# Kernel optimization log

Hardware: AMD Instinct MI355X
Metric: run time of the kernel (lower is better)

The kernel has to match this reference:

```python
import jax, jax.numpy as jnp
import numpy as np

N_ENT = 50000     # n_entities
C = 128           # channel
N_EDGES = 1600000 # n_edges (avg degree 32)
N_REL = 11        # n_relations; edge_type in [1, N_REL-1]
N_HOPS = 3
EPS = 1e-12       # F.normalize default eps


def setup_inputs() -> dict:
    key = jax.random.key(0)
    k1, k2, k3, k4 = jax.random.split(key, 4)
    entity_emb = jax.random.normal(k1, (N_ENT, C), dtype=jnp.float32)
    edge_index = jax.random.randint(k2, (2, N_EDGES), 0, N_ENT, dtype=jnp.int64)
    edge_type = jax.random.randint(k3, (N_EDGES,), 1, N_REL, dtype=jnp.int64)
    # xavier_uniform bound for (N_REL-1, C)
    bound = float(np.sqrt(6.0 / ((N_REL - 1) + C)))
    weight = jax.random.uniform(k4, (N_REL - 1, C), jnp.float32, -bound, bound)
    return {"entity_emb": entity_emb, "edge_index": edge_index,
            "edge_type": edge_type, "weight": weight}


def reference(entity_emb, edge_index, edge_type, weight):
    head, tail = edge_index[0], edge_index[1]
    # relation embedding per edge: weight[edge_type - 1] -> [E, C]
    rel_emb = weight[edge_type - 1]
    ones = jnp.ones((edge_index.shape[1],), entity_emb.dtype)
    # per-head in-degree counts (constant across hops)
    cnt = jax.ops.segment_sum(ones, head, num_segments=N_ENT)
    denom = jnp.maximum(cnt, 1.0)[:, None]  # scatter_mean: zero rows stay zero

    def hop(emb):
        msg = emb[tail] * rel_emb                                   # gather + mul [E, C]
        agg = jax.ops.segment_sum(msg, head, num_segments=N_ENT) / denom  # scatter_mean
        # F.normalize (L2 per row)
        norm = jnp.linalg.norm(agg, axis=1, keepdims=True)
        return agg / jnp.maximum(norm, EPS)

    res = entity_emb
    emb = entity_emb
    for _ in range(N_HOPS):
        emb = hop(emb)
        res = res + emb
    return res
```

## Files before the change

### kernel.cpp

```cpp
#include <hip/hip_runtime.h>

#define N_ENT   50000
#define CH      128
#define N_EDGES 1600000
#define N_RELM1 10
#define NB      391
#define BCAP    4608
#define PART_BLOCKS 512
#define PART_CHUNK  ((N_EDGES + PART_BLOCKS - 1) / PART_BLOCKS)
#define SUBCAP  40
#define EPS_N   1e-12f

__device__ __forceinline__ unsigned int f2bf_bits(float f) {
    unsigned int x = __float_as_uint(f);
    return (x + 0x7FFFu + ((x >> 16) & 1u)) >> 16;
}

__global__ void gc_cvt_kernel(const float* __restrict__ ent,
                              unsigned int* __restrict__ emb) {
    int i = blockIdx.x * blockDim.x + threadIdx.x;
    if (i < N_ENT * (CH / 2)) {
        float2 v = *(const float2*)(ent + 2 * (size_t)i);
        emb[i] = f2bf_bits(v.x) | (f2bf_bits(v.y) << 16);
    }
}

__global__ __launch_bounds__(256) void gc_part_kernel(const int* __restrict__ head,
                                                      const int* __restrict__ tail,
                                                      const int* __restrict__ etyp,
                                                      int* __restrict__ barr,
                                                      int* __restrict__ cnts) {
    __shared__ int ctr[NB];
    int tid = threadIdx.x;
    for (int i = tid; i < NB; i += 256) ctr[i] = 0;
    __syncthreads();
    int lo = blockIdx.x * PART_CHUNK;
    int hi = min(lo + PART_CHUNK, N_EDGES);
    size_t gbase = (size_t)blockIdx.x * NB * SUBCAP;
    for (int e = lo + tid; e < hi; e += 256) {
        int h = head[e];
        int b = h >> 7;
        int slot = atomicAdd(&ctr[b], 1);
        if (slot < SUBCAP)
            barr[gbase + (size_t)b * SUBCAP + slot] =
                (tail[e] & 0xFFFF) | ((etyp[e] - 1) << 16) | ((h & 127) << 20);
    }
    __syncthreads();
    for (int i = tid; i < NB; i += 256)
        cnts[blockIdx.x * NB + i] = min(ctr[i], SUBCAP);
}

__global__ __launch_bounds__(256) void gc_place_kernel(const int* __restrict__ barr,
                                                       const int* __restrict__ cnts,
                                                       unsigned int* __restrict__ off_deg,
                                                       int* __restrict__ csr) {
    __shared__ int ent_s[BCAP];
    __shared__ int gcnt[PART_BLOCKS];
    __shared__ int goff[PART_BLOCKS + 1];
    __shared__ int hcnt[128];
    __shared__ int hloc[128];
    __shared__ int hctr[128];
    int b = blockIdx.x, tid = threadIdx.x;
    if (tid < 128) { hcnt[tid] = 0; hctr[tid] = 0; }
    for (int g = tid; g < PART_BLOCKS; g += 256) gcnt[g] = cnts[g * NB + b];
    __syncthreads();
    if (tid < 64) {
        int base = tid * 8;
        int loc[8];
        int s = 0;
        #pragma unroll
        for (int k = 0; k < 8; ++k) { loc[k] = s; s += gcnt[base + k]; }
        int x = s;
        #pragma unroll
        for (int d = 1; d < 64; d <<= 1) {
            int y = __shfl_up(x, d, 64);
            if (tid >= d) x += y;
        }
        int excl = x - s;
        #pragma unroll
        for (int k = 0; k < 8; ++k) goff[base + k] = excl + loc[k];
        if (tid == 63) goff[PART_BLOCKS] = excl + s;
    }
    __syncthreads();
    int n = goff[PART_BLOCKS];
    for (int g = tid; g < PART_BLOCKS; g += 256) {
        int c = gcnt[g];
        size_t src = ((size_t)g * NB + b) * SUBCAP;
        int dstl = goff[g];
        for (int k = 0; k < c; ++k) ent_s[dstl + k] = barr[src + k];
    }
    __syncthreads();
    for (int i = tid; i < n; i += 256)
        atomicAdd(&hcnt[(ent_s[i] >> 20) & 127], 1);
    __syncthreads();
    int v = (tid < 128) ? hcnt[tid] : 0;
    for (int d = 1; d < 128; d <<= 1) {
        int t = (tid < 128 && tid >= d) ? hcnt[tid - d] : 0;
        __syncthreads();
        if (tid < 128) hcnt[tid] += t;
        __syncthreads();
    }
    int lo = b * BCAP;
    if (tid < 128) {
        int start = lo + hcnt[tid] - v;
        hloc[tid] = start;
        int h = (b << 7) + tid;
        if (h < N_ENT) off_deg[h] = ((unsigned)start << 11) | (unsigned)v;
    }
    __syncthreads();
    for (int i = tid; i < n; i += 256) {
        int e = ent_s[i];
        int hl = (e >> 20) & 127;
        int pos = hloc[hl] + atomicAdd(&hctr[hl], 1);
        csr[pos] = e & 0xFFFFF;
    }
}

__global__ __launch_bounds__(256) void gc_hop_kernel(
        const unsigned int* __restrict__ src,
        const unsigned int* __restrict__ off_deg,
        const int* __restrict__ csr,
        const float* __restrict__ wt,
        unsigned int* __restrict__ dst,
        float* __restrict__ res,
        const float* __restrict__ ent,
        int init) {
    __shared__ float wt_s[N_RELM1 * CH];
    for (int i = threadIdx.x; i < N_RELM1 * CH; i += 256) wt_s[i] = wt[i];
    __syncthreads();

    int wave = threadIdx.x >> 6, lane = threadIdx.x & 63;
    int row = __builtin_amdgcn_readfirstlane(blockIdx.x * 4 + wave);

    unsigned od = (unsigned)__builtin_amdgcn_readfirstlane((int)off_deg[row]);
    int seg = (int)(od >> 11);
    int deg = (int)(od & 2047u);
    int seg_end = seg + deg;

    float ax = 0.f, ay = 0.f;
    int j = seg;
    for (; j + 8 <= seg_end; j += 8) {
        int pk[8];
        #pragma unroll
        for (int u = 0; u < 8; ++u)
            pk[u] = __builtin_amdgcn_readfirstlane(csr[j + u]);
        #pragma unroll
        for (int u = 0; u < 8; ++u) {
            unsigned v = src[pk[u] % 65536 * 64 + lane];
            float2 w = *(const float2*)(&wt_s[(pk[u] >> 16) * CH + 2 * lane]);
            ax = fmaf(__uint_as_float(v << 16), w.x, ax);
            ay = fmaf(__uint_as_float(v & 0xFFFF0000u), w.y, ay);
        }
    }
    for (; j < seg_end; ++j) {
        int pk = __builtin_amdgcn_readfirstlane(csr[j]);
        unsigned v = src[pk % 65536 * 64 + lane];
        float2 w = *(const float2*)(&wt_s[(pk >> 16) * CH + 2 * lane]);
        ax = fmaf(__uint_as_float(v << 16), w.x, ax);
        ay = fmaf(__uint_as_float(v & 0xFFFF0000u), w.y, ay);
    }

    float invd = 1.0f / fmaxf((float)deg, 1.0f);
    float x0 = ax * invd, x1 = ay * invd;

    float s = x0 * x0 + x1 * x1;
    #pragma unroll
    for (int o = 32; o > 0; o >>= 1) s += __shfl_down(s, o, 64);
    s = __shfl(s, 0, 64);

    float inv = 1.0f / fmaxf(sqrtf(s), EPS_N);
    float y0 = x0 * inv, y1 = x1 * inv;

    dst[(row << 6) + lane] = f2bf_bits(y0) | (f2bf_bits(y1) << 16);

    int base = (row << 7) + 2 * lane;
    if (init) {
        float2 e = *(const float2*)(ent + base);
        *(float2*)(res + base) = make_float2(e.x + y0, e.y + y1);
    } else {
        float2 rv = *(const float2*)(res + base);
        *(float2*)(res + base) = make_float2(rv.x + y0, rv.y + y1);
    }
}

extern "C" void kernel_launch(void* const* d_in, const int* in_sizes, int n_in,
                              void* d_out, int out_size, void* d_ws, size_t ws_size,
                              hipStream_t stream) {
    const float* ent  = (const float*)d_in[0];
    const int*   eidx = (const int*)d_in[1];
    const int*   etyp = (const int*)d_in[2];
    const float* wt   = (const float*)d_in[3];
    float*       res  = (float*)d_out;

    const int* head = eidx;
    const int* tail = eidx + N_EDGES;

    unsigned int* embA = (unsigned int*)d_ws;
    unsigned int* embB = embA + (size_t)N_ENT * 64;
    int* barr = (int*)(embB + (size_t)N_ENT * 64);
    int* cnts = barr + (size_t)PART_BLOCKS * NB * SUBCAP;
    unsigned int* off_deg = (unsigned int*)(cnts + PART_BLOCKS * NB);
    int* csr  = (int*)(off_deg + N_ENT);

    gc_part_kernel<<<PART_BLOCKS, 256, 0, stream>>>(head, tail, etyp, barr, cnts);
    gc_place_kernel<<<NB, 256, 0, stream>>>(barr, cnts, off_deg, csr);
    gc_cvt_kernel<<<(N_ENT * 64 + 255) / 256, 256, 0, stream>>>(ent, embA);

    const int hop_grid = N_ENT / 4;
    gc_hop_kernel<<<hop_grid, 256, 0, stream>>>(embA, off_deg, csr, wt, embB, res, ent, 1);
    gc_hop_kernel<<<hop_grid, 256, 0, stream>>>(embB, off_deg, csr, wt, embA, res, ent, 0);
    gc_hop_kernel<<<hop_grid, 256, 0, stream>>>(embA, off_deg, csr, wt, embB, res, ent, 0);
}
```

Baseline: 304.0 us.

## Fuse bf16 conversion into partition kernel and sort CSR by tail sub-bucket

The separate fp32-to-bf16 conversion kernel is folded into the partition kernel as a grid-stride tail loop, which removes one launch. The place kernel now runs with 512 threads, one per partition block, and uses a block-wide prefix scan with vectorised int4 copies from the bucket array. Edges within each head are also sorted by a 3-bit key taken from tail bits, so gathers in the hop kernels touch nearby embedding rows. The costs are extra scan passes and more shared memory in the place kernel, and the int4 loads may read past each sub-bucket's valid count.

```diff
diff --git a/kernel.cpp b/kernel.cpp
--- a/kernel.cpp
+++ b/kernel.cpp
@@ -9,27 +9,21 @@
 #define PART_BLOCKS 512
 #define PART_CHUNK  ((N_EDGES + PART_BLOCKS - 1) / PART_BLOCKS)
 #define SUBCAP  40
+#define NSL     8
 #define EPS_N   1e-12f
 
 __device__ __forceinline__ unsigned int f2bf_bits(float f) {
     unsigned int x = __float_as_uint(f);
     return (x + 0x7FFFu + ((x >> 16) & 1u)) >> 16;
-}
-
-__global__ void gc_cvt_kernel(const float* __restrict__ ent,
-                              unsigned int* __restrict__ emb) {
-    int i = blockIdx.x * blockDim.x + threadIdx.x;
-    if (i < N_ENT * (CH / 2)) {
-        float2 v = *(const float2*)(ent + 2 * (size_t)i);
-        emb[i] = f2bf_bits(v.x) | (f2bf_bits(v.y) << 16);
-    }
 }
 
 __global__ __launch_bounds__(256) void gc_part_kernel(const int* __restrict__ head,
                                                       const int* __restrict__ tail,
                                                       const int* __restrict__ etyp,
                                                       int* __restrict__ barr,
-                                                      int* __restrict__ cnts) {
+                                                      int* __restrict__ cnts,
+                                                      const float* __restrict__ ent,
+                                                      unsigned int* __restrict__ emb) {
     __shared__ int ctr[NB];
     int tid = threadIdx.x;
     for (int i = tid; i < NB; i += 256) ctr[i] = 0;
@@ -48,70 +42,76 @@
     __syncthreads();
     for (int i = tid; i < NB; i += 256)
         cnts[blockIdx.x * NB + i] = min(ctr[i], SUBCAP);
-}
-
-__global__ __launch_bounds__(256) void gc_place_kernel(const int* __restrict__ barr,
+    for (int i = blockIdx.x * 256 + tid; i < N_ENT * (CH / 2); i += PART_BLOCKS * 256) {
+        float2 v = *(const float2*)(ent + 2 * (size_t)i);
+        emb[i] = f2bf_bits(v.x) | (f2bf_bits(v.y) << 16);
+    }
+}
+
+__global__ __launch_bounds__(512) void gc_place_kernel(const int* __restrict__ barr,
                                                        const int* __restrict__ cnts,
                                                        unsigned int* __restrict__ off_deg,
                                                        int* __restrict__ csr) {
     __shared__ int ent_s[BCAP];
-    __shared__ int gcnt[PART_BLOCKS];
-    __shared__ int goff[PART_BLOCKS + 1];
-    __shared__ int hcnt[128];
-    __shared__ int hloc[128];
-    __shared__ int hctr[128];
+    __shared__ int kcnt[128 * NSL];
+    __shared__ int kloc[128 * NSL];
+    __shared__ int kctr[128 * NSL];
+    __shared__ int psum[512];
     int b = blockIdx.x, tid = threadIdx.x;
-    if (tid < 128) { hcnt[tid] = 0; hctr[tid] = 0; }
-    for (int g = tid; g < PART_BLOCKS; g += 256) gcnt[g] = cnts[g * NB + b];
-    __syncthreads();
-    if (tid < 64) {
-        int base = tid * 8;
-        int loc[8];
-        int s = 0;
-        #pragma unroll
-        for (int k = 0; k < 8; ++k) { loc[k] = s; s += gcnt[base + k]; }
-        int x = s;
-        #pragma unroll
-        for (int d = 1; d < 64; d <<= 1) {
-            int y = __shfl_up(x, d, 64);
-            if (tid >= d) x += y;
-        }
-        int excl = x - s;
-        #pragma unroll
-        for (int k = 0; k < 8; ++k) goff[base + k] = excl + loc[k];
-        if (tid == 63) goff[PART_BLOCKS] = excl + s;
-    }
-    __syncthreads();
-    int n = goff[PART_BLOCKS];
-    for (int g = tid; g < PART_BLOCKS; g += 256) {
-        int c = gcnt[g];
-        size_t src = ((size_t)g * NB + b) * SUBCAP;
-        int dstl = goff[g];
-        for (int k = 0; k < c; ++k) ent_s[dstl + k] = barr[src + k];
-    }
-    __syncthreads();
-    for (int i = tid; i < n; i += 256)
-        atomicAdd(&hcnt[(ent_s[i] >> 20) & 127], 1);
-    __syncthreads();
-    int v = (tid < 128) ? hcnt[tid] : 0;
-    for (int d = 1; d < 128; d <<= 1) {
-        int t = (tid < 128 && tid >= d) ? hcnt[tid - d] : 0;
-        __syncthreads();
-        if (tid < 128) hcnt[tid] += t;
-        __syncthreads();
-    }
+    for (int i = tid; i < 128 * NSL; i += 512) { kcnt[i] = 0; kctr[i] = 0; }
+    int c = cnts[tid * NB + b];
+    psum[tid] = c;
+    __syncthreads();
+    for (int d = 1; d < 512; d <<= 1) {
+        int t = (tid >= d) ? psum[tid - d] : 0;
+        __syncthreads();
+        psum[tid] += t;
+        __syncthreads();
+    }
+    int my_off = psum[tid] - c;
+    int n = psum[511];
+    size_t src = ((size_t)tid * NB + b) * SUBCAP;
+    for (int k = 0; k < c; k += 4) {
+        int4 v = *(const int4*)(barr + src + k);
+        ent_s[my_off + k] = v.x;
+        if (k + 1 < c) ent_s[my_off + k + 1] = v.y;
+        if (k + 2 < c) ent_s[my_off + k + 2] = v.z;
+        if (k + 3 < c) ent_s[my_off + k + 3] = v.w;
+    }
+    __syncthreads();
+    for (int i = tid; i < n; i += 512) {
+        int e = ent_s[i];
+        int key = (((e >> 20) & 127) << 3) | ((e >> 13) & 7);
+        atomicAdd(&kcnt[key], 1);
+    }
+    __syncthreads();
+    int a0 = kcnt[2 * tid], a1 = kcnt[2 * tid + 1];
+    int s2 = a0 + a1;
+    psum[tid] = s2;
+    __syncthreads();
+    for (int d = 1; d < 512; d <<= 1) {
+        int t = (tid >= d) ? psum[tid - d] : 0;
+        __syncthreads();
+        psum[tid] += t;
+        __syncthreads();
+    }
+    int excl = psum[tid] - s2;
+    kloc[2 * tid] = excl;
+    kloc[2 * tid + 1] = excl + a0;
+    __syncthreads();
     int lo = b * BCAP;
     if (tid < 128) {
-        int start = lo + hcnt[tid] - v;
-        hloc[tid] = start;
+        int start = kloc[tid * NSL];
+        int end_ = (tid == 127) ? n : kloc[(tid + 1) * NSL];
         int h = (b << 7) + tid;
-        if (h < N_ENT) off_deg[h] = ((unsigned)start << 11) | (unsigned)v;
-    }
-    __syncthreads();
-    for (int i = tid; i < n; i += 256) {
+        if (h < N_ENT)
+            off_deg[h] = ((unsigned)(lo + start) << 11) | (unsigned)(end_ - start);
+    }
+    __syncthreads();
+    for (int i = tid; i < n; i += 512) {
         int e = ent_s[i];
-        int hl = (e >> 20) & 127;
-        int pos = hloc[hl] + atomicAdd(&hctr[hl], 1);
+        int key = (((e >> 20) & 127) << 3) | ((e >> 13) & 7);
+        int pos = lo + kloc[key] + atomicAdd(&kctr[key], 1);
         csr[pos] = e & 0xFFFFF;
     }
 }
@@ -202,9 +202,8 @@
     unsigned int* off_deg = (unsigned int*)(cnts + PART_BLOCKS * NB);
     int* csr  = (int*)(off_deg + N_ENT);
 
-    gc_part_kernel<<<PART_BLOCKS, 256, 0, stream>>>(head, tail, etyp, barr, cnts);
-    gc_place_kernel<<<NB, 256, 0, stream>>>(barr, cnts, off_deg, csr);
-    gc_cvt_kernel<<<(N_ENT * 64 + 255) / 256, 256, 0, stream>>>(ent, embA);
+    gc_part_kernel<<<PART_BLOCKS, 256, 0, stream>>>(head, tail, etyp, barr, cnts, ent, embA);
+    gc_place_kernel<<<NB, 512, 0, stream>>>(barr, cnts, off_deg, csr);
 
     const int hop_grid = N_ENT / 4;
     gc_hop_kernel<<<hop_grid, 256, 0, stream>>>(embA, off_deg, csr, wt, embB, res, ent, 1);
```

Measured after the change: 300.7 us. No clear change (-1.1%).
